# Kernel tuning notes

Measured on AMD Instinct MI355X. Metric: run time of the kernel, lower is better.

## Reference

```python
import jax, jax.numpy as jnp
import numpy as np
from jax import lax

EPS = 1e-5  # BatchNorm eps (inference mode: running_mean=m, running_var=v)
DN = ('NCDHW', 'OIDHW', 'NCDHW')


def _conv_bn_relu(x, W, b, g, bt, m, v, pad):
    y = lax.conv_general_dilated(x, W, window_strides=(1, 1, 1), padding=pad,
                                 dimension_numbers=DN)
    y = y + b[None, :, None, None, None]
    scale = g / jnp.sqrt(v + EPS)
    y = (y - m[None, :, None, None, None]) * scale[None, :, None, None, None] \
        + bt[None, :, None, None, None]
    return jax.nn.relu(y)


def _cal_patt(k, q, v):
    # spatial non-local attention over H*W, independently per (n, c, d)
    N, C, D, H, W = q.shape
    qf = q.reshape(N, C, D, H * W)
    kf = k.reshape(N, C, D, H * W)
    vf = v.reshape(N, C, D, H * W)
    # sigma[n,c,d,i,j] = q_i * k_j ; softmax over j ; out[j] = sum_i v_i * r_ij
    sigma = qf[..., :, None] * kf[..., None, :]          # [N,C,D,HW,HW]
    r = jax.nn.softmax(sigma, axis=-1)
    out = jnp.einsum('ncdi,ncdij->ncdj', vf, r)
    return out.reshape(N, C, D, H, W)


def _cal_datt(k, q, v):
    # temporal non-local attention over D, independently per (n, c, h, w)
    N, C, D, H, W = q.shape
    qf = jnp.transpose(q, (0, 1, 3, 4, 2))               # [N,C,H,W,D]
    kf = jnp.transpose(k, (0, 1, 3, 4, 2))
    vf = jnp.transpose(v, (0, 1, 3, 4, 2))
    sigma = qf[..., :, None] * kf[..., None, :]          # [N,C,H,W,D,D]
    r = jax.nn.softmax(sigma, axis=-1)
    out = jnp.einsum('nchwi,nchwij->nchwj', vf, r)
    return jnp.transpose(out, (0, 1, 4, 2, 3))           # back to [N,C,D,H,W]


def setup_inputs() -> dict:
    key = jax.random.key(0)
    ks = jax.random.split(key, 8)
    C, Cc = 512, 64  # features_, features_//compress
    N, D, H, W = 2, 8, 16, 16
    f32 = jnp.float32

    def bn(c):
        return (jnp.ones((c,), f32), jnp.zeros((c,), f32),
                jnp.zeros((c,), f32), jnp.ones((c,), f32))

    x = jax.random.normal(ks[0], (N, C, D, H, W), f32)
    Wq = jax.random.normal(ks[1], (Cc, C, 1, 1, 1), f32) * 0.04
    Wk = jax.random.normal(ks[2], (Cc, C, 1, 1, 1), f32) * 0.04
    Wv = jax.random.normal(ks[3], (Cc, C, 1, 1, 1), f32) * 0.04
    Ws = jax.random.normal(ks[4], (C, Cc, 3, 3, 3), f32) * 0.02
    Wd = jax.random.normal(ks[5], (C, Cc, 3, 3, 3), f32) * 0.02
    gq, btq, mq, vq = bn(Cc)
    gk, btk, mk, vk = bn(Cc)
    gv, btv, mv, vv = bn(Cc)
    gs, bts, ms, vs = bn(C)
    gd, btd, md, vd = bn(C)
    return dict(
        x=x, gama=jnp.float32(0.5),
        Wq=Wq, bq=jnp.zeros((Cc,), f32), gq=gq, btq=btq, mq=mq, vq=vq,
        Wk=Wk, bk=jnp.zeros((Cc,), f32), gk=gk, btk=btk, mk=mk, vk=vk,
        Wv=Wv, bv=jnp.zeros((Cc,), f32), gv=gv, btv=btv, mv=mv, vv=vv,
        Ws=Ws, bs=jnp.zeros((C,), f32), gs=gs, bts=bts, ms=ms, vs=vs,
        Wd=Wd, bd=jnp.zeros((C,), f32), gd=gd, btd=btd, md=md, vd=vd,
    )


def reference(x, gama,
              Wq, bq, gq, btq, mq, vq,
              Wk, bk, gk, btk, mk, vk,
              Wv, bv, gv, btv, mv, vv,
              Ws, bs, gs, bts, ms, vs,
              Wd, bd, gd, btd, md, vd):
    P0 = [(0, 0)] * 3
    P1 = [(1, 1)] * 3
    v_x = _conv_bn_relu(x, Wv, bv, gv, btv, mv, vv, P0)
    k_x = _conv_bn_relu(x, Wk, bk, gk, btk, mk, vk, P0)
    q_x = _conv_bn_relu(x, Wq, bq, gq, btq, mq, vq, P0)
    # name == 'st': both spatial and temporal attention branches
    Patt = _cal_patt(k_x, q_x, v_x)
    Patt_c = _conv_bn_relu(Patt, Ws, bs, gs, bts, ms, vs, P1)
    Datt = _cal_datt(k_x, q_x, v_x)
    Datt_c = _conv_bn_relu(Datt, Wd, bd, gd, btd, md, vd, P1)
    return gama * (Datt_c + Patt_c) + x
```

## Files before the change

### kernel.cpp

```cpp
#include <hip/hip_runtime.h>
#include <cmath>

#define EPSBN 1e-5f

namespace {
constexpr int C_IN = 512;
constexpr int CC   = 64;
constexpr int CD   = 8;
constexpr int HW   = 256;
constexpr int DHW  = CD * HW;
constexpr int QSZ  = 2 * CC * DHW;

constexpr int PG    = 18 * 18;
constexpr int GPLN  = PG * 8;
constexpr int PADSZ = 2 * 10 * 8 * GPLN;
constexpr int WTSZ  = 27 * 512 * 64;

typedef __attribute__((ext_vector_type(8))) short bf16x8;
typedef __attribute__((ext_vector_type(4))) float f32x4;
typedef __attribute__((ext_vector_type(16))) float f32x16;

typedef unsigned int u32_g __attribute__((address_space(1)));
typedef unsigned int u32_l __attribute__((address_space(3)));

__device__ inline unsigned short f2bf(float f) {
    unsigned u = __float_as_uint(f);
    return (unsigned short)((u + 0x7fffu + ((u >> 16) & 1u)) >> 16);
}
}

__global__ __launch_bounds__(256) void prep_kernel(
    const float* __restrict__ Ws, const float* __restrict__ Wd,
    const float* __restrict__ Wq, const float* __restrict__ Wk,
    const float* __restrict__ Wv,
    const float* __restrict__ bs, const float* __restrict__ gs,
    const float* __restrict__ bts, const float* __restrict__ ms,
    const float* __restrict__ vs,
    const float* __restrict__ bd, const float* __restrict__ gd,
    const float* __restrict__ btd, const float* __restrict__ md,
    const float* __restrict__ vd,
    uint4* __restrict__ pads, unsigned short* __restrict__ Wt,
    unsigned short* __restrict__ Wqkv, float2* __restrict__ BNc)
{
    int bid = blockIdx.x;
    int t = threadIdx.x;
    if (bid < 405) {
        pads[bid * 256 + t] = make_uint4(0, 0, 0, 0);
    } else if (bid < 1429) {
        int b2 = bid - 405;
        int b  = b2 >> 9;
        int co = b2 & 511;
        const float* W = b ? Wd : Ws;
        int cog = co >> 6, co_l = co & 63;
        int r  = co_l & 31, hi = co_l >> 5;
        unsigned short* o = Wt + (size_t)b * WTSZ;
        for (int k = t; k < 27 * 64; k += 256) {
            int tap = k >> 6, ci = k & 63;
            int kd = tap / 9, tapk = tap - kd * 9;
            int half = ci >> 5, cl = ci & 31;
            int cig = cl >> 4, ci16 = cl & 15;
            int ks = ci16 >> 3;
            float w = W[((size_t)co * 64 + ci) * 27 + tap];
            int chunk = ((cog * 2 + half) * 3 + kd) * 2 + cig;
            int pg = (r * 2 + ks) ^ (r & 7);
            o[(size_t)chunk * 9216 + tapk * 1024 + hi * 512
              + pg * 8 + (ci16 & 7)] = f2bf(w);
        }
    } else if (bid < 1621) {
        int co = bid - 1429;
        const float* W = co < 64 ? Wq : co < 128 ? Wk : Wv;
        int c = co & 63;
        for (int ci = t; ci < 512; ci += 256)
            Wqkv[(size_t)co * 512 + ci] = f2bf(W[(size_t)c * 512 + ci]);
    } else {
        int gid = (bid - 1621) * 256 + t;
        if (gid < 1024) {
            int br = gid >> 9, co = gid & 511;
            float s, o;
            if (br == 0) {
                s = gs[co] * rsqrtf(vs[co] + EPSBN);
                o = (bs[co] - ms[co]) * s + bts[co];
            } else {
                s = gd[co] * rsqrtf(vd[co] + EPSBN);
                o = (bd[co] - md[co]) * s + btd[co];
            }
            BNc[gid] = make_float2(s, o);
        }
    }
}

__global__ __launch_bounds__(256) void qkv_gemm_kernel(
    const float* __restrict__ x, const unsigned short* __restrict__ Wqkv,
    const float* __restrict__ bq, const float* __restrict__ gq,
    const float* __restrict__ btq, const float* __restrict__ mq,
    const float* __restrict__ vq,
    const float* __restrict__ bk, const float* __restrict__ gk,
    const float* __restrict__ btk, const float* __restrict__ mk,
    const float* __restrict__ vk,
    const float* __restrict__ bv, const float* __restrict__ gv,
    const float* __restrict__ btv, const float* __restrict__ mv,
    const float* __restrict__ vv,
    float* __restrict__ outq, float* __restrict__ outk, float* __restrict__ outv)
{
    int bid = blockIdx.x;
    int n = bid >> 7, p0 = (bid & 127) * 16;

    __shared__ __align__(16) unsigned short xs[16 * 512];
    int t = threadIdx.x;

    const float* xb = x + ((size_t)n * C_IN) * DHW + p0;
#pragma unroll
    for (int pass = 0; pass < 8; ++pass) {
        int idx = pass * 256 + t;
        int ci = idx >> 2, pq = idx & 3;
        float4 v4 = *reinterpret_cast<const float4*>(xb + (size_t)ci * DHW + pq * 4);
        float arr[4] = {v4.x, v4.y, v4.z, v4.w};
#pragma unroll
        for (int u = 0; u < 4; ++u) {
            int pos = pq * 4 + u;
            int boff = pos * 1024 + ((ci * 2) ^ ((pos & 7) << 4));
            *reinterpret_cast<unsigned short*>(
                reinterpret_cast<char*>(xs) + boff) = f2bf(arr[u]);
        }
    }
    __syncthreads();

    int wid = t >> 6, lane = t & 63;
    int l15 = lane & 15, l4 = lane >> 4;
    int mh = wid * 3;
    int pos = l15;

    bf16x8 bfr[16];
    const char* xsb = reinterpret_cast<const char*>(xs) + pos * 1024;
    int swz = (pos & 7) << 4;
#pragma unroll
    for (int kk = 0; kk < 16; ++kk)
        bfr[kk] = *reinterpret_cast<const bf16x8*>(xsb + ((kk * 64 + l4 * 16) ^ swz));

    f32x4 acc[3];
#pragma unroll
    for (int i = 0; i < 3; ++i) acc[i] = (f32x4){0.f, 0.f, 0.f, 0.f};

#pragma unroll
    for (int i = 0; i < 3; ++i) {
        const unsigned short* wrow =
            Wqkv + ((size_t)(mh + i) * 16 + l15) * 512 + l4 * 8;
#pragma unroll
        for (int kk = 0; kk < 16; ++kk) {
            bf16x8 af = *reinterpret_cast<const bf16x8*>(wrow + kk * 32);
            acc[i] = __builtin_amdgcn_mfma_f32_16x16x32_bf16(af, bfr[kk], acc[i], 0, 0, 0);
        }
    }

#pragma unroll
    for (int i = 0; i < 3; ++i) {
        int mf = mh + i;
        int br = mf >> 2;
        const float* bb  = br == 0 ? bq  : br == 1 ? bk  : bv;
        const float* gg  = br == 0 ? gq  : br == 1 ? gk  : gv;
        const float* bt  = br == 0 ? btq : br == 1 ? btk : btv;
        const float* mm  = br == 0 ? mq  : br == 1 ? mk  : mv;
        const float* vvp = br == 0 ? vq  : br == 1 ? vk  : vv;
        float*       op  = br == 0 ? outq : br == 1 ? outk : outv;
        int cb = (mf & 3) * 16 + l4 * 4;
#pragma unroll
        for (int r = 0; r < 4; ++r) {
            int c = cb + r;
            float s = gg[c] * rsqrtf(vvp[c] + EPSBN);
            float val = (acc[i][r] + bb[c] - mm[c]) * s + bt[c];
            op[((size_t)(n * CC + c)) * DHW + p0 + pos] = fmaxf(val, 0.f);
        }
    }
}

__global__ __launch_bounds__(256) void att_kernel(
    const float* __restrict__ q, const float* __restrict__ k,
    const float* __restrict__ v,
    unsigned short* __restrict__ Pp, unsigned short* __restrict__ Dp)
{
    __shared__ float sk[256], sq[256], sw[256], red[4];
    int t = threadIdx.x;
    int bid = blockIdx.x;

    if (bid < 1024) {
        int n = bid >> 9, c = (bid >> 3) & 63, d = bid & 7;
        size_t base = (size_t)bid * HW;
        float kt = k[base + t];
        float qt = q[base + t];
        float vt = v[base + t];
        sk[t] = kt;
        sq[t] = qt;

        float m = kt;
#pragma unroll
        for (int off = 32; off >= 1; off >>= 1)
            m = fmaxf(m, __shfl_xor(m, off));
        if ((t & 63) == 0) red[t >> 6] = m;
        __syncthreads();
        float kmax = fmaxf(fmaxf(red[0], red[1]), fmaxf(red[2], red[3]));

        float qkm = qt * kmax;
        float d0 = 0.f, d1 = 0.f, d2 = 0.f, d3 = 0.f;
        for (int j = 0; j < 256; j += 4) {
            d0 += __expf(fmaf(qt, sk[j + 0], -qkm));
            d1 += __expf(fmaf(qt, sk[j + 1], -qkm));
            d2 += __expf(fmaf(qt, sk[j + 2], -qkm));
            d3 += __expf(fmaf(qt, sk[j + 3], -qkm));
        }
        float den = (d0 + d1) + (d2 + d3);
        sw[t] = vt / den;
        __syncthreads();

        float kjm = kt - kmax;
        float o0 = 0.f, o1 = 0.f, o2 = 0.f, o3 = 0.f;
        for (int i = 0; i < 256; i += 4) {
            o0 += sw[i + 0] * __expf(sq[i + 0] * kjm);
            o1 += sw[i + 1] * __expf(sq[i + 1] * kjm);
            o2 += sw[i + 2] * __expf(sq[i + 2] * kjm);
            o3 += sw[i + 3] * __expf(sq[i + 3] * kjm);
        }
        float o = (o0 + o1) + (o2 + o3);

        int h = t >> 4, w = t & 15;
        size_t dst = ((((size_t)(n * 10 + d + 1) * 8 + (c >> 3)) * PG)
                      + (h + 1) * 18 + (w + 1)) * 8 + (c & 7);
        Pp[dst] = f2bf(o);
    } else {
        int g = (bid - 1024) * 256 + t;
        int nc = g >> 8, hw = g & 255;
        int n = nc >> 6, c = nc & 63;
        size_t base = (size_t)nc * DHW + hw;

        float qv[8], kv[8], vv_[8];
#pragma unroll
        for (int d = 0; d < 8; ++d) {
            qv[d]  = q[base + d * HW];
            kv[d]  = k[base + d * HW];
            vv_[d] = v[base + d * HW];
        }
        float kmax = 0.f;
#pragma unroll
        for (int d = 0; d < 8; ++d) kmax = fmaxf(kmax, kv[d]);

        float wgt[8];
#pragma unroll
        for (int i = 0; i < 8; ++i) {
            float den = 0.f, qkm = qv[i] * kmax;
#pragma unroll
            for (int j = 0; j < 8; ++j)
                den += __expf(fmaf(qv[i], kv[j], -qkm));
            wgt[i] = vv_[i] / den;
        }
        int h = hw >> 4, w = hw & 15;
#pragma unroll
        for (int j = 0; j < 8; ++j) {
            float o = 0.f, kjm = kv[j] - kmax;
#pragma unroll
            for (int i = 0; i < 8; ++i)
                o += wgt[i] * __expf(qv[i] * kjm);
            size_t dst = ((((size_t)(n * 10 + j + 1) * 8 + (c >> 3)) * PG)
                          + (h + 1) * 18 + (w + 1)) * 8 + (c & 7);
            Dp[dst] = f2bf(o);
        }
    }
}

__global__ __launch_bounds__(256, 1) void conv_fused_kernel(
    const unsigned short* __restrict__ Pp, const unsigned short* __restrict__ Dp,
    const unsigned short* __restrict__ Wt,
    const float2* __restrict__ BNc,
    const float* __restrict__ x, const float* __restrict__ gama,
    float* __restrict__ out)
{
    int bid = blockIdx.x;
    int cog = bid & 7;
    int pgb = (bid >> 3) & 1;
    int sl  = bid >> 4;
    int n = sl >> 3, d = sl & 7;

    __shared__ __align__(16) unsigned short lds_in[24 * 1536];
    __shared__ __align__(16) unsigned short lds_w[2 * 18432];

    int t = threadIdx.x;
    int wid = t >> 6, lane = t & 63;
    int ph = wid & 1, br = wid >> 1;
    int col  = lane & 31;
    int wcol = lane & 15;
    int hl   = (lane >> 4) & 1;
    int ks   = lane >> 5;
    int gA   = ((col * 2 + ks) ^ (col & 7)) * 8;

    f32x16 acc[2][2];
#pragma unroll
    for (int m = 0; m < 2; ++m)
#pragma unroll
        for (int p = 0; p < 2; ++p)
#pragma unroll
            for (int r = 0; r < 16; ++r)
                acc[m][p][r] = 0.f;

#define ISTAGE(hf_) do {                                                      \
    _Pragma("unroll")                                                         \
    for (int pc = 0; pc < 24; ++pc) {                                         \
        const unsigned short* sb = ((pc >= 12) ? Dp : Pp)                     \
            + ((size_t)((n * 10 + d + ((pc % 12) >> 2)) * 8 + (hf_) * 4       \
                        + ((pc % 12) & 3))) * GPLN + pgb * 1152;              \
        _Pragma("unroll")                                                     \
        for (int j = 0; j < 3; ++j) {                                         \
            if (((pc * 3 + j) & 3) == wid)                                    \
                __builtin_amdgcn_global_load_lds(                             \
                    (const u32_g*)(sb + j * 512 + lane * 8),                  \
                    (u32_l*)(lds_in + pc * 1536 + j * 512), 16, 0, 0);        \
        }                                                                     \
    }                                                                         \
} while (0)

#define DMAW(c_) do {                                                         \
    const int ch_ = (((cog * 2 + ((c_) / 6)) * 3 + (((c_) % 6) >> 1)) * 2     \
                     + ((c_) & 1)) * 9216;                                    \
    _Pragma("unroll")                                                         \
    for (int j = 0; j < 9; ++j) {                                             \
        int base = j * 2048 + wid * 512;                                      \
        const unsigned short* s0 = (base < 9216)                              \
            ? (Wt + ch_ + base)                                               \
            : (Wt + WTSZ + ch_ + (base - 9216));                              \
        __builtin_amdgcn_global_load_lds(                                     \
            (const u32_g*)(s0 + lane * 8),                                    \
            (u32_l*)(lds_w + ((c_) & 1) * 18432 + base), 16, 0, 0);           \
    }                                                                         \
} while (0)

#define COMPUTE(c_) do {                                                      \
    const int kd_ = ((c_) % 6) >> 1, cig_ = (c_) & 1;                         \
    const unsigned short* wb_ = lds_w + ((c_) & 1) * 18432 + br * 9216;       \
    const unsigned short* bp_ = lds_in + br * (12 * 1536)                     \
                                + (kd_ * 4 + cig_ * 2 + ks) * 1536;           \
    _Pragma("unroll")                                                         \
    for (int tapk = 0; tapk < 9; ++tapk) {                                    \
        const int kh_ = tapk / 3, kw_ = tapk % 3;                             \
        bf16x8 a0 = *(const bf16x8*)(wb_ + tapk * 1024 + gA);                 \
        bf16x8 a1 = *(const bf16x8*)(wb_ + tapk * 1024 + 512 + gA);           \
        bf16x8 b0 = *(const bf16x8*)(bp_ + ((ph * 4 + hl + kh_) * 18          \
                                     + wcol + kw_) * 8);                      \
        bf16x8 b1 = *(const bf16x8*)(bp_ + ((ph * 4 + 2 + hl + kh_) * 18      \
                                     + wcol + kw_) * 8);                      \
        acc[0][0] = __builtin_amdgcn_mfma_f32_32x32x16_bf16(a0, b0,           \
                        acc[0][0], 0, 0, 0);                                  \
        acc[0][1] = __builtin_amdgcn_mfma_f32_32x32x16_bf16(a0, b1,           \
                        acc[0][1], 0, 0, 0);                                  \
        acc[1][0] = __builtin_amdgcn_mfma_f32_32x32x16_bf16(a1, b0,           \
                        acc[1][0], 0, 0, 0);                                  \
        acc[1][1] = __builtin_amdgcn_mfma_f32_32x32x16_bf16(a1, b1,           \
                        acc[1][1], 0, 0, 0);                                  \
    }                                                                         \
} while (0)

    ISTAGE(0);
    DMAW(0);
    __syncthreads();

#pragma unroll
    for (int c = 0; c < 12; ++c) {
        if (c < 11) DMAW(c + 1);
        COMPUTE(c);
        __syncthreads();
        if (c == 5) {
            ISTAGE(1);
            __syncthreads();
        }
    }

#undef ISTAGE
#undef DMAW
#undef COMPUTE

    float gm = gama[0];
    float* ep = reinterpret_cast<float*>(lds_w);

    if (br == 0) {
#pragma unroll
        for (int m = 0; m < 2; ++m)
#pragma unroll
            for (int p = 0; p < 2; ++p)
#pragma unroll
                for (int r = 0; r < 16; ++r) {
                    int row = (r & 3) + 8 * (r >> 2) + 4 * ks;
                    float2 c2 = BNc[cog * 64 + m * 32 + row];
                    float v = fmaxf(acc[m][p][r] * c2.x + c2.y, 0.f);
                    ep[ph * 4096 + (m * 32 + row) * 64 + p * 32 + col] = v;
                }
    }
    __syncthreads();
    if (br == 1) {
#pragma unroll
        for (int m = 0; m < 2; ++m)
#pragma unroll
            for (int p = 0; p < 2; ++p)
#pragma unroll
                for (int r = 0; r < 16; ++r) {
                    int row = (r & 3) + 8 * (r >> 2) + 4 * ks;
                    int co = cog * 64 + m * 32 + row;
                    float2 c2 = BNc[512 + co];
                    float rd = fmaxf(acc[m][p][r] * c2.x + c2.y, 0.f);
                    float rp = ep[ph * 4096 + (m * 32 + row) * 64 + p * 32 + col];
                    int pos = pgb * 128 + ph * 64 + p * 32 + col;
                    size_t oi = ((size_t)(n * 512 + co)) * 2048 + d * 256 + pos;
                    out[oi] = gm * (rp + rd) + x[oi];
                }
    }
}

extern "C" void kernel_launch(void* const* d_in, const int* in_sizes, int n_in,
                              void* d_out, int out_size, void* d_ws, size_t ws_size,
                              hipStream_t stream)
{
    const float* x    = (const float*)d_in[0];
    const float* gama = (const float*)d_in[1];
    const float* Wq  = (const float*)d_in[2];
    const float* bq  = (const float*)d_in[3];
    const float* gq  = (const float*)d_in[4];
    const float* btq = (const float*)d_in[5];
    const float* mq  = (const float*)d_in[6];
    const float* vq  = (const float*)d_in[7];
    const float* Wk  = (const float*)d_in[8];
    const float* bk  = (const float*)d_in[9];
    const float* gk  = (const float*)d_in[10];
    const float* btk = (const float*)d_in[11];
    const float* mk  = (const float*)d_in[12];
    const float* vk  = (const float*)d_in[13];
    const float* Wv  = (const float*)d_in[14];
    const float* bv  = (const float*)d_in[15];
    const float* gv  = (const float*)d_in[16];
    const float* btv = (const float*)d_in[17];
    const float* mv  = (const float*)d_in[18];
    const float* vv  = (const float*)d_in[19];
    const float* Ws  = (const float*)d_in[20];
    const float* bs  = (const float*)d_in[21];
    const float* gs  = (const float*)d_in[22];
    const float* bts = (const float*)d_in[23];
    const float* ms  = (const float*)d_in[24];
    const float* vs  = (const float*)d_in[25];
    const float* Wd  = (const float*)d_in[26];
    const float* bd  = (const float*)d_in[27];
    const float* gd  = (const float*)d_in[28];
    const float* btd = (const float*)d_in[29];
    const float* md  = (const float*)d_in[30];
    const float* vd  = (const float*)d_in[31];

    char* ws = (char*)d_ws;
    unsigned short* Pp   = (unsigned short*)ws;
    unsigned short* Dp   = Pp + PADSZ;
    unsigned short* Wt   = Dp + PADSZ;
    unsigned short* Wqkv = Wt + 2 * WTSZ;
    float* q = (float*)(ws + 5394432);
    float* k = q + QSZ;
    float* v = k + QSZ;
    float2* BNc = (float2*)(ws + 5394432 + 3 * 1048576);

    prep_kernel<<<1625, 256, 0, stream>>>(
        Ws, Wd, Wq, Wk, Wv,
        bs, gs, bts, ms, vs,
        bd, gd, btd, md, vd,
        (uint4*)Pp, Wt, Wqkv, BNc);

    qkv_gemm_kernel<<<256, 256, 0, stream>>>(
        x, Wqkv,
        bq, gq, btq, mq, vq,
        bk, gk, btk, mk, vk,
        bv, gv, btv, mv, vv,
        q, k, v);

    att_kernel<<<1152, 256, 0, stream>>>(q, k, v, Pp, Dp);

    conv_fused_kernel<<<256, 256, 0, stream>>>(
        Pp, Dp, Wt, BNc,
        x, gama, (float*)d_out);
}
```

Baseline: 65.02 us.

## Move conv weight repack into attention kernel and use exp2 with vectorized LDS

The 3x3x3 conv weight reorder and the BN constant computation move out of the prep kernel into extra blocks of the attention kernel. This shrinks the serial prep launch and lets that work overlap with attention compute. The weight reorder now reads the source contiguously (co*1728 + k2) for coalesced loads. The spatial softmax loops pre-scale q by log2(e) and call the hardware exp2 directly, and they read LDS as float4 with unrolling to cut instruction count. The attention kernel now carries more parameters and a larger grid.

```diff
diff --git a/kernel.cpp b/kernel.cpp
--- a/kernel.cpp
+++ b/kernel.cpp
@@ -15,6 +15,7 @@
 constexpr int GPLN  = PG * 8;
 constexpr int PADSZ = 2 * 10 * 8 * GPLN;
 constexpr int WTSZ  = 27 * 512 * 64;
+constexpr float LOG2E = 1.44269504088896f;
 
 typedef __attribute__((ext_vector_type(8))) short bf16x8;
 typedef __attribute__((ext_vector_type(4))) float f32x4;
@@ -29,63 +30,21 @@
 }
 }
 
-__global__ __launch_bounds__(256) void prep_kernel(
-    const float* __restrict__ Ws, const float* __restrict__ Wd,
+__global__ __launch_bounds__(256) void prep_small_kernel(
     const float* __restrict__ Wq, const float* __restrict__ Wk,
-    const float* __restrict__ Wv,
-    const float* __restrict__ bs, const float* __restrict__ gs,
-    const float* __restrict__ bts, const float* __restrict__ ms,
-    const float* __restrict__ vs,
-    const float* __restrict__ bd, const float* __restrict__ gd,
-    const float* __restrict__ btd, const float* __restrict__ md,
-    const float* __restrict__ vd,
-    uint4* __restrict__ pads, unsigned short* __restrict__ Wt,
-    unsigned short* __restrict__ Wqkv, float2* __restrict__ BNc)
+    const float* __restrict__ Wv, unsigned short* __restrict__ Wqkv,
+    uint4* __restrict__ pads)
 {
     int bid = blockIdx.x;
     int t = threadIdx.x;
-    if (bid < 405) {
-        pads[bid * 256 + t] = make_uint4(0, 0, 0, 0);
-    } else if (bid < 1429) {
-        int b2 = bid - 405;
-        int b  = b2 >> 9;
-        int co = b2 & 511;
-        const float* W = b ? Wd : Ws;
-        int cog = co >> 6, co_l = co & 63;
-        int r  = co_l & 31, hi = co_l >> 5;
-        unsigned short* o = Wt + (size_t)b * WTSZ;
-        for (int k = t; k < 27 * 64; k += 256) {
-            int tap = k >> 6, ci = k & 63;
-            int kd = tap / 9, tapk = tap - kd * 9;
-            int half = ci >> 5, cl = ci & 31;
-            int cig = cl >> 4, ci16 = cl & 15;
-            int ks = ci16 >> 3;
-            float w = W[((size_t)co * 64 + ci) * 27 + tap];
-            int chunk = ((cog * 2 + half) * 3 + kd) * 2 + cig;
-            int pg = (r * 2 + ks) ^ (r & 7);
-            o[(size_t)chunk * 9216 + tapk * 1024 + hi * 512
-              + pg * 8 + (ci16 & 7)] = f2bf(w);
-        }
-    } else if (bid < 1621) {
-        int co = bid - 1429;
+    if (bid < 192) {
+        int co = bid;
         const float* W = co < 64 ? Wq : co < 128 ? Wk : Wv;
         int c = co & 63;
         for (int ci = t; ci < 512; ci += 256)
             Wqkv[(size_t)co * 512 + ci] = f2bf(W[(size_t)c * 512 + ci]);
     } else {
-        int gid = (bid - 1621) * 256 + t;
-        if (gid < 1024) {
-            int br = gid >> 9, co = gid & 511;
-            float s, o;
-            if (br == 0) {
-                s = gs[co] * rsqrtf(vs[co] + EPSBN);
-                o = (bs[co] - ms[co]) * s + bts[co];
-            } else {
-                s = gd[co] * rsqrtf(vd[co] + EPSBN);
-                o = (bd[co] - md[co]) * s + btd[co];
-            }
-            BNc[gid] = make_float2(s, o);
-        }
+        pads[(bid - 192) * 256 + t] = make_uint4(0, 0, 0, 0);
     }
 }
 
@@ -176,9 +135,18 @@
 __global__ __launch_bounds__(256) void att_kernel(
     const float* __restrict__ q, const float* __restrict__ k,
     const float* __restrict__ v,
-    unsigned short* __restrict__ Pp, unsigned short* __restrict__ Dp)
+    const float* __restrict__ Ws, const float* __restrict__ Wd,
+    const float* __restrict__ bs, const float* __restrict__ gs,
+    const float* __restrict__ bts, const float* __restrict__ ms,
+    const float* __restrict__ vs,
+    const float* __restrict__ bd, const float* __restrict__ gd,
+    const float* __restrict__ btd, const float* __restrict__ md,
+    const float* __restrict__ vd,
+    unsigned short* __restrict__ Pp, unsigned short* __restrict__ Dp,
+    unsigned short* __restrict__ Wt, float2* __restrict__ BNc)
 {
-    __shared__ float sk[256], sq[256], sw[256], red[4];
+    __shared__ __align__(16) float sk[256], sq2[256], sw[256];
+    __shared__ float red[4];
     int t = threadIdx.x;
     int bid = blockIdx.x;
 
@@ -188,8 +156,9 @@
         float kt = k[base + t];
         float qt = q[base + t];
         float vt = v[base + t];
-        sk[t] = kt;
-        sq[t] = qt;
+        float qt2 = qt * LOG2E;
+        sk[t]  = kt;
+        sq2[t] = qt2;
 
         float m = kt;
 #pragma unroll
@@ -199,13 +168,16 @@
         __syncthreads();
         float kmax = fmaxf(fmaxf(red[0], red[1]), fmaxf(red[2], red[3]));
 
-        float qkm = qt * kmax;
+        float qkm2 = qt2 * kmax;
         float d0 = 0.f, d1 = 0.f, d2 = 0.f, d3 = 0.f;
-        for (int j = 0; j < 256; j += 4) {
-            d0 += __expf(fmaf(qt, sk[j + 0], -qkm));
-            d1 += __expf(fmaf(qt, sk[j + 1], -qkm));
-            d2 += __expf(fmaf(qt, sk[j + 2], -qkm));
-            d3 += __expf(fmaf(qt, sk[j + 3], -qkm));
+        const float4* sk4 = reinterpret_cast<const float4*>(sk);
+#pragma unroll 8
+        for (int j = 0; j < 64; ++j) {
+            float4 kk = sk4[j];
+            d0 += __builtin_amdgcn_exp2f(fmaf(qt2, kk.x, -qkm2));
+            d1 += __builtin_amdgcn_exp2f(fmaf(qt2, kk.y, -qkm2));
+            d2 += __builtin_amdgcn_exp2f(fmaf(qt2, kk.z, -qkm2));
+            d3 += __builtin_amdgcn_exp2f(fmaf(qt2, kk.w, -qkm2));
         }
         float den = (d0 + d1) + (d2 + d3);
         sw[t] = vt / den;
@@ -213,11 +185,16 @@
 
         float kjm = kt - kmax;
         float o0 = 0.f, o1 = 0.f, o2 = 0.f, o3 = 0.f;
-        for (int i = 0; i < 256; i += 4) {
-            o0 += sw[i + 0] * __expf(sq[i + 0] * kjm);
-            o1 += sw[i + 1] * __expf(sq[i + 1] * kjm);
-            o2 += sw[i + 2] * __expf(sq[i + 2] * kjm);
-            o3 += sw[i + 3] * __expf(sq[i + 3] * kjm);
+        const float4* sw4 = reinterpret_cast<const float4*>(sw);
+        const float4* sq4 = reinterpret_cast<const float4*>(sq2);
+#pragma unroll 8
+        for (int i = 0; i < 64; ++i) {
+            float4 ww = sw4[i];
+            float4 qq = sq4[i];
+            o0 += ww.x * __builtin_amdgcn_exp2f(qq.x * kjm);
+            o1 += ww.y * __builtin_amdgcn_exp2f(qq.y * kjm);
+            o2 += ww.z * __builtin_amdgcn_exp2f(qq.z * kjm);
+            o3 += ww.w * __builtin_amdgcn_exp2f(qq.w * kjm);
         }
         float o = (o0 + o1) + (o2 + o3);
 
@@ -225,7 +202,7 @@
         size_t dst = ((((size_t)(n * 10 + d + 1) * 8 + (c >> 3)) * PG)
                       + (h + 1) * 18 + (w + 1)) * 8 + (c & 7);
         Pp[dst] = f2bf(o);
-    } else {
+    } else if (bid < 1152) {
         int g = (bid - 1024) * 256 + t;
         int nc = g >> 8, hw = g & 255;
         int n = nc >> 6, c = nc & 63;
@@ -261,6 +238,41 @@
             size_t dst = ((((size_t)(n * 10 + j + 1) * 8 + (c >> 3)) * PG)
                           + (h + 1) * 18 + (w + 1)) * 8 + (c & 7);
             Dp[dst] = f2bf(o);
+        }
+    } else if (bid < 2176) {
+        int b2 = bid - 1152;
+        int b  = b2 >> 9;
+        int co = b2 & 511;
+        const float* W = b ? Wd : Ws;
+        int cog = co >> 6, co_l = co & 63;
+        int r  = co_l & 31, hi = co_l >> 5;
+        unsigned short* o = Wt + (size_t)b * WTSZ;
+        for (int k2 = t; k2 < 27 * 64; k2 += 256) {
+            int ci  = k2 / 27;
+            int tap = k2 - ci * 27;
+            int kd = tap / 9, tapk = tap - kd * 9;
+            int half = ci >> 5, cl = ci & 31;
+            int cig = cl >> 4, ci16 = cl & 15;
+            int ks = ci16 >> 3;
+            float w = W[(size_t)co * 1728 + k2];
+            int chunk = ((cog * 2 + half) * 3 + kd) * 2 + cig;
+            int pg = (r * 2 + ks) ^ (r & 7);
+            o[(size_t)chunk * 9216 + tapk * 1024 + hi * 512
+              + pg * 8 + (ci16 & 7)] = f2bf(w);
+        }
+    } else {
+        int gid = (bid - 2176) * 256 + t;
+        if (gid < 1024) {
+            int br = gid >> 9, co = gid & 511;
+            float s, o;
+            if (br == 0) {
+                s = gs[co] * rsqrtf(vs[co] + EPSBN);
+                o = (bs[co] - ms[co]) * s + bts[co];
+            } else {
+                s = gd[co] * rsqrtf(vd[co] + EPSBN);
+                o = (bd[co] - md[co]) * s + btd[co];
+            }
+            BNc[gid] = make_float2(s, o);
         }
     }
 }
@@ -457,11 +469,7 @@
     float* v = k + QSZ;
     float2* BNc = (float2*)(ws + 5394432 + 3 * 1048576);
 
-    prep_kernel<<<1625, 256, 0, stream>>>(
-        Ws, Wd, Wq, Wk, Wv,
-        bs, gs, bts, ms, vs,
-        bd, gd, btd, md, vd,
-        (uint4*)Pp, Wt, Wqkv, BNc);
+    prep_small_kernel<<<597, 256, 0, stream>>>(Wq, Wk, Wv, Wqkv, (uint4*)Pp);
 
     qkv_gemm_kernel<<<256, 256, 0, stream>>>(
         x, Wqkv,
@@ -470,7 +478,12 @@
         bv, gv, btv, mv, vv,
         q, k, v);
 
-    att_kernel<<<1152, 256, 0, stream>>>(q, k, v, Pp, Dp);
+    att_kernel<<<2180, 256, 0, stream>>>(
+        q, k, v,
+        Ws, Wd,
+        bs, gs, bts, ms, vs,
+        bd, gd, btd, md, vd,
+        Pp, Dp, Wt, BNc);
 
     conv_fused_kernel<<<256, 256, 0, stream>>>(
         Pp, Dp, Wt, BNc,
```

After: 66.11 us. About the same (+1.7%).
